# Optimization experiments

Hardware: AMD Instinct MI355X
Metric: run time of the kernel (lower is better)

Reference implementation:

```python
import jax, jax.numpy as jnp
import numpy as np
from jax import lax

L, B, T_IMG, T_TXT = 12, 2, 256, 64
E, H, G = 1024, 16, 2730
V = 16416  # image_vocab_count + 1
C = E // H
EPS = 1e-6  # flax LayerNorm default


def _ln(x, scale, bias):
    mu = jnp.mean(x, -1, keepdims=True)
    var = jnp.var(x, -1, keepdims=True)
    y = (x - mu) * lax.rsqrt(var + EPS)
    if scale is not None:
        y = y * scale
    if bias is not None:
        y = y + bias
    return y


def _attend(k, v, q, mask, o_w):
    # k,v: [B,K,H,C]  q: [B,Q,H,C]  mask: [B,K]
    bias = jnp.where(mask, 0.0, -jnp.inf)[:, None, None, :]
    w = jnp.einsum('bqhc,bkhc->bhqk', q, k) + bias
    w = jax.nn.softmax(w, axis=-1)
    out = jnp.einsum('bhqk,bkhc->bqhc', w, v)
    return out.reshape(out.shape[0], out.shape[1], E) @ o_w


def setup_inputs():
    key = jax.random.key(0)
    ks = jax.random.split(key, 16)
    s = 0.02
    n = lambda k, shape: jax.random.normal(k, shape, jnp.float32) * s
    return dict(
        encoder_state=n(ks[0], (B, T_TXT, E)),
        keys_state=jnp.zeros((L, B, T_IMG, H, C), jnp.float32),
        values_state=jnp.zeros((L, B, T_IMG, H, C), jnp.float32),
        attention_mask=jnp.ones((B, T_TXT), jnp.bool_),
        prev_token=5000,
        token_index=100,
        embed_tok=n(ks[1], (V, E)),
        embed_pos=n(ks[2], (T_IMG, E)),
        ln_emb_s=jnp.ones((E,), jnp.float32),
        ln_emb_b=jnp.zeros((E,), jnp.float32),
        final_ln_b=jnp.zeros((E,), jnp.float32),
        lm_head_w=n(ks[3], (E, V)),
        pre_sa_ln_b=jnp.zeros((L, E), jnp.float32),
        sa_q_w=n(ks[4], (L, E, E)), sa_k_w=n(ks[5], (L, E, E)),
        sa_v_w=n(ks[6], (L, E, E)), sa_o_w=n(ks[7], (L, E, E)),
        sa_ln_s=jnp.ones((L, E), jnp.float32), sa_ln_b=jnp.zeros((L, E), jnp.float32),
        pre_ca_ln_b=jnp.zeros((L, E), jnp.float32),
        ca_q_w=n(ks[8], (L, E, E)), ca_k_w=n(ks[9], (L, E, E)),
        ca_v_w=n(ks[10], (L, E, E)), ca_o_w=n(ks[11], (L, E, E)),
        ca_ln_s=jnp.ones((L, E), jnp.float32), ca_ln_b=jnp.zeros((L, E), jnp.float32),
        glu_ln0_b=jnp.zeros((L, E), jnp.float32),
        glu_fc0_w=n(ks[12], (L, E, G)), glu_fc1_w=n(ks[13], (L, E, G)),
        glu_ln1_b=jnp.zeros((L, G), jnp.float32),
        glu_fc2_w=n(ks[14], (L, G, E)),
    )


def _decode_step(encoder_state, keys_state, values_state, attention_mask,
                 prev_token, token_index, embed_tok, embed_pos,
                 ln_emb_s, ln_emb_b, final_ln_b, lm_head_w, layer_params):
    ones = jnp.ones((B, 1), jnp.int32)
    ds = embed_tok[prev_token * ones] + embed_pos[token_index * ones]  # [B,1,E]
    ds = _ln(ds, ln_emb_s, ln_emb_b)
    self_mask = jnp.broadcast_to(jnp.arange(T_IMG) < token_index + 1, (B, T_IMG))
    scale = C ** 0.5

    def step(ds, xs):
        ks_l, vs_l, p = xs  # per-layer KV cache [B,T_IMG,H,C] and params
        (pre_sa_b, qw, kw, vw, ow, sa_s, sa_b,
         pre_ca_b, cqw, ckw, cvw, cow, ca_s, ca_b,
         g0b, f0, f1, g1b, f2) = p
        # --- self attention with KV-cache append ---
        residual = ds
        x = _ln(ds, None, pre_sa_b)
        ks_l = lax.dynamic_update_slice(ks_l, (x @ kw).reshape(B, 1, H, C), (0, token_index, 0, 0))
        vs_l = lax.dynamic_update_slice(vs_l, (x @ vw).reshape(B, 1, H, C), (0, token_index, 0, 0))
        q = (x @ qw).reshape(B, 1, H, C) / scale
        x = _attend(ks_l, vs_l, q, self_mask, ow)
        ds = residual + _ln(x, sa_s, sa_b)
        # --- cross attention over encoder state ---
        residual = ds
        x = _ln(ds, None, pre_ca_b)
        ek = (encoder_state @ ckw).reshape(B, T_TXT, H, C)
        ev = (encoder_state @ cvw).reshape(B, T_TXT, H, C)
        q = (x @ cqw).reshape(B, 1, H, C) / scale
        x = _attend(ek, ev, q, attention_mask, cow)
        ds = residual + _ln(x, ca_s, ca_b)
        # --- GLU FFN ---
        residual = ds
        z = _ln(ds, None, g0b)
        w = jax.nn.gelu(z @ f0, approximate=False)
        z = _ln(w * (z @ f1), None, g1b)
        ds = residual + z @ f2
        return ds, (ks_l, vs_l)

    ds, (keys_state, values_state) = lax.scan(step, ds, (keys_state, values_state, layer_params))
    ds = _ln(ds, None, final_ln_b)
    logits = ds @ lm_head_w  # [B,1,V]
    return logits, keys_state, values_state


def reference(encoder_state, keys_state, values_state, attention_mask, prev_token,
              token_index, embed_tok, embed_pos, ln_emb_s, ln_emb_b, final_ln_b,
              lm_head_w, pre_sa_ln_b, sa_q_w, sa_k_w, sa_v_w, sa_o_w, sa_ln_s,
              sa_ln_b, pre_ca_ln_b, ca_q_w, ca_k_w, ca_v_w, ca_o_w, ca_ln_s,
              ca_ln_b, glu_ln0_b, glu_fc0_w, glu_fc1_w, glu_ln1_b, glu_fc2_w):
    layer_params = (pre_sa_ln_b, sa_q_w, sa_k_w, sa_v_w, sa_o_w, sa_ln_s, sa_ln_b,
                    pre_ca_ln_b, ca_q_w, ca_k_w, ca_v_w, ca_o_w, ca_ln_s, ca_ln_b,
                    glu_ln0_b, glu_fc0_w, glu_fc1_w, glu_ln1_b, glu_fc2_w)
    return _decode_step(encoder_state, keys_state, values_state, attention_mask,
                        prev_token, token_index, embed_tok, embed_pos,
                        ln_emb_s, ln_emb_b, final_ln_b, lm_head_w, layer_params)
```

## Files before the change

kernel.cpp:

```cpp
#include <hip/hip_runtime.h>
#include <math.h>

#define LAYERS 12
#define EE 1024
#define GG 2730
#define VV 16416
#define EPS 1e-6f

#define OFF_DS 0
#define NSLOT 37
#define OFF_ACC (OFF_DS + NSLOT*2048)
#define ACC_STRIDE 28672
#define AQ 0
#define AK 2048
#define AV 4096
#define AY 6144
#define ASC 10240
#define AOUT 12288
#define AY2 14336
#define AA 16384
#define AB2 21844
#define ACC_TOTAL (LAYERS*ACC_STRIDE)
#define ZERO_FLOATS (NSLOT*2048 + ACC_TOTAL)

#define KVL 524288
#define KVB 262144

struct MegaP {
  const float* enc; const float* keys_in; const float* values_in;
  const int* maski; const int* pt; const int* ti;
  const float* tok; const float* pos; const float* ln_s; const float* ln_b;
  const float* final_b; const float* lm_w;
  const float* pre_sa_b; const float* saq; const float* sak; const float* sav;
  const float* sao; const float* sas; const float* sab;
  const float* pre_ca_b; const float* caq; const float* ckw; const float* cvw;
  const float* cao; const float* cas; const float* cab;
  const float* g0b; const float* f0; const float* f1; const float* g1b; const float* f2;
  float* logits; float* keys_out; float* values_out; float* ws;
};

__device__ __forceinline__ void red4(float* sm, float& a, float& b, float& c, float& d){
  #pragma unroll
  for(int o=32;o;o>>=1){ a+=__shfl_down(a,o); b+=__shfl_down(b,o); c+=__shfl_down(c,o); d+=__shfl_down(d,o); }
  int w=threadIdx.x>>6, l=threadIdx.x&63;
  __syncthreads();
  if(l==0){ sm[w]=a; sm[4+w]=b; sm[8+w]=c; sm[12+w]=d; }
  __syncthreads();
  a=sm[0]+sm[1]+sm[2]+sm[3]; b=sm[4]+sm[5]+sm[6]+sm[7];
  c=sm[8]+sm[9]+sm[10]+sm[11]; d=sm[12]+sm[13]+sm[14]+sm[15];
}

__device__ __forceinline__ void ln_stats_g(const float* v, int K, float* sm,
    float& mu0, float& rs0, float& mu1, float& rs1){
  float s0=0,q0=0,s1=0,q1=0;
  for(int i=threadIdx.x;i<K;i+=256){ float a=v[i], b=v[K+i]; s0+=a;q0+=a*a;s1+=b;q1+=b*b; }
  red4(sm,s0,q0,s1,q1);
  mu0=s0/K; mu1=s1/K;
  rs0=rsqrtf(fmaxf(q0/K-mu0*mu0,0.f)+EPS);
  rs1=rsqrtf(fmaxf(q1/K-mu1*mu1,0.f)+EPS);
}

__device__ __forceinline__ void ln_stats_l(float (*Ds)[1024], float* sm,
    float& mu0, float& rs0, float& mu1, float& rs1){
  float s0=0,q0=0,s1=0,q1=0;
  for(int i=threadIdx.x;i<EE;i+=256){ float a=Ds[0][i], b=Ds[1][i]; s0+=a;q0+=a*a;s1+=b;q1+=b*b; }
  red4(sm,s0,q0,s1,q1);
  mu0=s0/EE; mu1=s1/EE;
  rs0=rsqrtf(fmaxf(q0/EE-mu0*mu0,0.f)+EPS);
  rs1=rsqrtf(fmaxf(q1/EE-mu1*mu1,0.f)+EPS);
}

__device__ __forceinline__ void build_ds3(const float* dsi, const float* accL,
    const float* sasl, const float* sabl, const float* casl, const float* cabl,
    float (*Ds)[1024], float* sm){
  float mu0,rs0,mu1,rs1;
  ln_stats_g(accL+AY, EE, sm, mu0,rs0,mu1,rs1);
  for(int i=threadIdx.x;i<EE;i+=256){ float sc=sasl[i], bi=sabl[i];
    Ds[0][i]=dsi[i]    + (accL[AY+i]-mu0)*rs0*sc + bi;
    Ds[1][i]=dsi[EE+i] + (accL[AY+EE+i]-mu1)*rs1*sc + bi; }
  ln_stats_g(accL+AY2, EE, sm, mu0,rs0,mu1,rs1);
  for(int i=threadIdx.x;i<EE;i+=256){ float sc=casl[i], bi=cabl[i];
    Ds[0][i] += (accL[AY2+i]-mu0)*rs0*sc + bi;
    Ds[1][i] += (accL[AY2+EE+i]-mu1)*rs1*sc + bi; }
}

__global__ __launch_bounds__(256)
void k_prelude(MegaP p){
  __shared__ float ev[EE];
  __shared__ float sm[16];
  const int t=threadIdx.x;
  int ptv = p.pt[0], tiv = p.ti[0];
  float s0=0,q0=0,d1=0,d2=0;
  for(int i=t;i<EE;i+=256){ float v=p.tok[(size_t)ptv*EE+i]+p.pos[(size_t)tiv*EE+i]; ev[i]=v; s0+=v; q0+=v*v; }
  red4(sm,s0,q0,d1,d2);
  float mu=s0/EE, rs=rsqrtf(fmaxf(q0/EE-mu*mu,0.f)+EPS);
  float* ds0 = p.ws + OFF_DS;
  __syncthreads();
  for(int i=t;i<EE;i+=256){ float y=(ev[i]-mu)*rs*p.ln_s[i]+p.ln_b[i]; ds0[i]=y; ds0[EE+i]=y; }
}

__global__ __launch_bounds__(256)
void k_qkv(MegaP p, int l){
  __shared__ float Xs[2][1024];
  __shared__ float sm[16];
  const int t=threadIdx.x, bx=blockIdx.x, by=blockIdx.y;
  if (bx >= 12){
    int cb = (bx-12)*64 + by;
    #pragma unroll
    for(int j=0;j<4;j++){
      int idx4 = cb*1024 + j*256 + t;
      int kv = idx4 >> 17;
      int r4 = idx4 & 131071;
      size_t off = (size_t)l*KVL + (size_t)r4*4;
      float4 v = *(const float4*)((kv? p.values_in : p.keys_in) + off);
      *(float4*)((kv? p.values_out : p.keys_out) + off) = v;
    }
    return;
  }
  const float* dsi = p.ws + OFF_DS + (size_t)(3*l)*2048;
  float* accL = p.ws + OFF_ACC + (size_t)l*ACC_STRIDE;
  const size_t lE2=(size_t)l*EE*EE, lE=(size_t)l*EE;
  int c = bx*256 + t;
  int sel = c>>10, cc = c&1023;
  const float* W = (sel==0? p.saq : sel==1? p.sak : p.sav) + lE2;
  float* O = accL + (sel==0? AQ : sel==1? AK : AV);
  int k0 = by*16;
  const float* wp = W + (size_t)k0*EE + cc;
  float wr[16];
  #pragma unroll
  for(int k=0;k<16;k++) wr[k] = wp[(size_t)k*EE];
  float mu0,rs0,mu1,rs1;
  ln_stats_g(dsi, EE, sm, mu0,rs0,mu1,rs1);
  for(int i=t;i<EE;i+=256){ float bi=p.pre_sa_b[lE+i];
    Xs[0][i]=(dsi[i]-mu0)*rs0+bi; Xs[1][i]=(dsi[EE+i]-mu1)*rs1+bi; }
  __syncthreads();
  float a0=0,a1=0;
  #pragma unroll
  for(int k=0;k<16;k++){ a0+=Xs[0][k0+k]*wr[k]; a1+=Xs[1][k0+k]*wr[k]; }
  atomicAdd(&O[cc],a0); atomicAdd(&O[EE+cc],a1);
}

__global__ __launch_bounds__(256)
void k_selfo(MegaP p, int l){
  __shared__ float Ds[2][1024];
  __shared__ float att[2][256];
  __shared__ float sm[16];
  const int t=threadIdx.x, bkid=blockIdx.x, tiv=p.ti[0];
  float* accL = p.ws + OFF_ACC + (size_t)l*ACC_STRIDE;
  const size_t lE2=(size_t)l*EE*EE;
  int cg=bkid&3, h=(bkid>>2)&15, sub=(bkid>>6)&3, hoff=h*64;
  if (t < 128){ int bb2=t>>6, c2=t&63; Ds[bb2][c2] = accL[AQ + bb2*EE + hoff + c2]*0.125f; }
  __syncthreads();
  for(int bb2=0;bb2<2;bb2++)
    for(int tt=t; tt<=tiv; tt+=256){
      const float* kr = (tt<tiv) ? (p.keys_in + (size_t)l*KVL + (size_t)bb2*KVB + (size_t)tt*EE + hoff)
                                 : (accL + AK + bb2*EE + hoff);
      float d=0;
      #pragma unroll
      for(int c2=0;c2<64;c2++) d += Ds[bb2][c2]*kr[c2];
      att[bb2][tt] = d;
    }
  __syncthreads();
  int wv=t>>6, l2=t&63;
  if (wv<2){
    float m=-3.4e38f;
    for(int tt=l2; tt<=tiv; tt+=64) m=fmaxf(m, att[wv][tt]);
    #pragma unroll
    for(int o=32;o;o>>=1) m=fmaxf(m,__shfl_xor(m,o));
    float s=0;
    for(int tt=l2; tt<=tiv; tt+=64){ float e=__expf(att[wv][tt]-m); att[wv][tt]=e; s+=e; }
    #pragma unroll
    for(int o=32;o;o>>=1) s+=__shfl_xor(s,o);
    if(l2==0) sm[8+wv]=1.f/s;
  }
  __syncthreads();
  {
    int bb2=t>>7, j=(t>>3)&15, part=t&7, colh=sub*16+j;
    float v=0;
    for(int tt=part; tt<=tiv; tt+=8){
      float vv = (tt<tiv)? p.values_in[(size_t)l*KVL + (size_t)bb2*KVB + (size_t)tt*EE + hoff + colh]
                         : accL[AV + bb2*EE + hoff + colh];
      v += att[bb2][tt]*vv;
    }
    v += __shfl_down(v,4,8); v += __shfl_down(v,2,8); v += __shfl_down(v,1,8);
    if(part==0) Ds[bb2][512+j] = v*sm[8+bb2];
  }
  __syncthreads();
  {
    int c = cg*256+t, kb = hoff + sub*16;
    const float* wp = p.sao + lE2 + (size_t)kb*EE + c;
    float a0=0,a1=0;
    #pragma unroll
    for(int j2=0;j2<16;j2++){ float w=wp[(size_t)j2*EE]; a0+=Ds[0][512+j2]*w; a1+=Ds[1][512+j2]*w; }
    atomicAdd(&accL[AY+c],a0); atomicAdd(&accL[AY+EE+c],a1);
  }
  if (cg==0 && sub==0){
    int bb2=t>>7, kv=(t>>6)&1, c2=t&63;
    float val = accL[(kv?AV:AK) + bb2*EE + hoff + c2];
    float* dst = (kv? p.values_out : p.keys_out)
               + (size_t)l*KVL + (size_t)bb2*KVB + (size_t)tiv*EE + hoff + c2;
    *dst = val;
  }
}

__global__ __launch_bounds__(256)
void k_qscore(MegaP p, int l){
  __shared__ float Xs[1024];
  __shared__ float P[16][64];
  __shared__ float qs[64];
  __shared__ float us[256];
  __shared__ float sm[16];
  const int t=threadIdx.x, bh=blockIdx.x, ec=blockIdx.y;
  const int b=bh>>4, h=bh&15, hoff=h*64;
  float* accL = p.ws + OFF_ACC + (size_t)l*ACC_STRIDE;
  const float* dsi = p.ws + OFF_DS + (size_t)(3*l)*2048;
  const size_t lE2=(size_t)l*EE*EE, lE=(size_t)l*EE;
  const int w=t>>6, ln=t&63;

  float s0=0,q0=0;
  for(int i=t;i<EE;i+=256){ float v=accL[AY+b*EE+i]; s0+=v; q0+=v*v; }
  #pragma unroll
  for(int o=32;o;o>>=1){ s0+=__shfl_down(s0,o); q0+=__shfl_down(q0,o); }
  if(ln==0){ sm[w]=s0; sm[4+w]=q0; }
  __syncthreads();
  float mu=(sm[0]+sm[1]+sm[2]+sm[3])/EE;
  float qq=(sm[4]+sm[5]+sm[6]+sm[7])/EE;
  float rs=rsqrtf(fmaxf(qq-mu*mu,0.f)+EPS);
  float s1=0,q1=0;
  for(int i=t;i<EE;i+=256){
    float d = dsi[b*EE+i] + (accL[AY+b*EE+i]-mu)*rs*p.sas[lE+i] + p.sab[lE+i];
    Xs[i]=d; s1+=d; q1+=d*d;
  }
  #pragma unroll
  for(int o=32;o;o>>=1){ s1+=__shfl_down(s1,o); q1+=__shfl_down(q1,o); }
  if(ln==0){ sm[8+w]=s1; sm[12+w]=q1; }
  __syncthreads();
  float mu2=(sm[8]+sm[9]+sm[10]+sm[11])/EE;
  float q2=(sm[12]+sm[13]+sm[14]+sm[15])/EE;
  float rs2=rsqrtf(fmaxf(q2-mu2*mu2,0.f)+EPS);
  for(int i=t;i<EE;i+=256) Xs[i] = (Xs[i]-mu2)*rs2 + p.pre_ca_b[lE+i];
  __syncthreads();

  {
    int c4=t&15, kr=t>>4;
    const float4* cq = (const float4*)(p.caq + lE2 + (size_t)kr*EE + hoff) + c4;
    float ax=0,ay=0,az=0,aw=0;
    #pragma unroll 8
    for(int i=0;i<64;i++){
      float4 wv = cq[(size_t)i*16*256];
      float x = Xs[kr+16*i];
      ax+=x*wv.x; ay+=x*wv.y; az+=x*wv.z; aw+=x*wv.w;
    }
    P[kr][c4*4+0]=ax; P[kr][c4*4+1]=ay; P[kr][c4*4+2]=az; P[kr][c4*4+3]=aw;
  }
  __syncthreads();
  if (t<64){
    float qv=0;
    #pragma unroll
    for(int kr=0;kr<16;kr++) qv += P[kr][t];
    qs[t] = qv*0.125f;
  }
  __syncthreads();

  {
    const float4* ckp = (const float4*)(p.ckw + lE2 + (size_t)(ec*256+t)*EE + hoff);
    float u=0;
    #pragma unroll
    for(int j=0;j<16;j++){
      float4 wv=ckp[j];
      u += wv.x*qs[4*j] + wv.y*qs[4*j+1] + wv.z*qs[4*j+2] + wv.w*qs[4*j+3];
    }
    us[t]=u;
  }
  __syncthreads();

  int t2=t&63, q4=t>>6;
  const float4* ep = (const float4*)(p.enc + (size_t)(b*64+t2)*EE + ec*256 + q4*64);
  float pa=0;
  #pragma unroll
  for(int j=0;j<16;j++){
    float4 e4=ep[j];
    pa += e4.x*us[q4*64+4*j] + e4.y*us[q4*64+4*j+1] + e4.z*us[q4*64+4*j+2] + e4.w*us[q4*64+4*j+3];
  }
  atomicAdd(&accL[ASC + (b*16+h)*64 + t2], pa);
}

__global__ __launch_bounds__(256)
void k_ov(MegaP p, int l){
  __shared__ float att[64];
  __shared__ float ctxp[2][128];
  __shared__ float ctxs[128];
  __shared__ float smr[2];
  const int t=threadIdx.x, bh=blockIdx.x, es=blockIdx.y;
  const int b=bh>>4, h=bh&15, hoff=h*64, e0=es*128;
  float* accL = p.ws + OFF_ACC + (size_t)l*ACC_STRIDE;
  const size_t lE2=(size_t)l*EE*EE;
  const int c=t&63, part=t>>6;
  const float* vp = p.cvw + lE2 + (size_t)(e0+part*32)*EE + hoff + c;
  float wr[32];
  #pragma unroll
  for(int j=0;j<32;j++) wr[j] = vp[(size_t)j*EE];
  if (t<64){
    float sc = accL[ASC + (b*16+h)*64 + t];
    int mi=b*64+t;
    bool valid = (p.maski[mi]!=0) || (((const unsigned char*)p.maski)[mi]!=0);
    sc = valid? sc : -3.4e38f;
    float m=sc;
    #pragma unroll
    for(int o=32;o;o>>=1) m=fmaxf(m,__shfl_xor(m,o));
    float e_ = valid? __expf(sc-m) : 0.f;
    float s=e_;
    #pragma unroll
    for(int o=32;o;o>>=1) s+=__shfl_xor(s,o);
    att[t]=e_;
    if(t==0) smr[0]=1.f/s;
  }
  __syncthreads();
  {
    int e2=t>>1, half=t&1;
    const float* ep = p.enc + (size_t)(b*64+half*32)*EE + e0+e2;
    float ca=0;
    #pragma unroll 8
    for(int tt=0;tt<32;tt++) ca += att[half*32+tt]*ep[(size_t)tt*EE];
    ctxp[half][e2]=ca;
  }
  __syncthreads();
  if (t<128) ctxs[t] = (ctxp[0][t]+ctxp[1][t])*smr[0];
  __syncthreads();
  float a=0;
  #pragma unroll
  for(int j=0;j<32;j++) a += ctxs[part*32+j]*wr[j];
  atomicAdd(&accL[AOUT + b*EE + hoff + c], a);
}

__global__ __launch_bounds__(256)
void k_y2(MegaP p, int l){
  __shared__ float Xs[2][1024];
  const int t=threadIdx.x;
  float* accL = p.ws + OFF_ACC + (size_t)l*ACC_STRIDE;
  const size_t lE2=(size_t)l*EE*EE;
  int c = blockIdx.x*256 + t;
  int k0 = blockIdx.y*16;
  const float* wp = p.cao + lE2 + (size_t)k0*EE + c;
  float wr[16];
  #pragma unroll
  for(int k=0;k<16;k++) wr[k] = wp[(size_t)k*EE];
  for(int i=t;i<EE;i+=256){ Xs[0][i]=accL[AOUT+i]; Xs[1][i]=accL[AOUT+EE+i]; }
  __syncthreads();
  float a0=0,a1=0;
  #pragma unroll
  for(int k=0;k<16;k++){ a0+=Xs[0][k0+k]*wr[k]; a1+=Xs[1][k0+k]*wr[k]; }
  atomicAdd(&accL[AY2+c],a0); atomicAdd(&accL[AY2+EE+c],a1);
}

__global__ __launch_bounds__(256)
void k_glu01(MegaP p, int l){
  __shared__ float Xs[2][1024];
  __shared__ float Ds[2][1024];
  __shared__ float sm[16];
  const int t=threadIdx.x;
  const float* dsi = p.ws + OFF_DS + (size_t)(3*l)*2048;
  float* accL = p.ws + OFF_ACC + (size_t)l*ACC_STRIDE;
  const size_t lEG=(size_t)l*EE*GG, lE=(size_t)l*EE;
  int c2 = blockIdx.x*256 + t;
  int k0 = blockIdx.y*16;
  int sel=0, col=0;
  const float* W = nullptr;
  float2 wr[16];
  if (c2 < 2730){
    sel = (c2>=1365); int cc2 = sel? c2-1365 : c2; col = cc2*2;
    W = (sel? p.f1 : p.f0) + lEG;
    const float2* wp = (const float2*)(W + (size_t)k0*GG + col);
    #pragma unroll
    for(int k=0;k<16;k++) wr[k] = wp[(size_t)k*1365];
  }
  build_ds3(dsi, accL, p.sas+lE, p.sab+lE, p.cas+lE, p.cab+lE, Ds, sm);
  float mu0,rs0,mu1,rs1;
  ln_stats_l(Ds, sm, mu0,rs0,mu1,rs1);
  for(int i=t;i<EE;i+=256){ float bi=p.g0b[lE+i];
    Xs[0][i]=(Ds[0][i]-mu0)*rs0+bi; Xs[1][i]=(Ds[1][i]-mu1)*rs1+bi; }
  __syncthreads();
  if (c2 < 2730){
    float* O = accL + (sel? AB2 : AA);
    float a0=0,a1=0,b0=0,b1=0;
    #pragma unroll
    for(int k=0;k<16;k++){
      float x0=Xs[0][k0+k], x1=Xs[1][k0+k];
      a0+=x0*wr[k].x; a1+=x0*wr[k].y; b0+=x1*wr[k].x; b1+=x1*wr[k].y;
    }
    atomicAdd(&O[col+0],a0); atomicAdd(&O[col+1],a1);
    atomicAdd(&O[GG+col+0],b0); atomicAdd(&O[GG+col+1],b1);
  }
}

__global__ __launch_bounds__(256)
void k_glu2(MegaP p, int l){
  __shared__ float Xs[2][2736];
  __shared__ float Ds[2][1024];
  __shared__ float sm[16];
  const int t=threadIdx.x;
  const float* dsi = p.ws + OFF_DS + (size_t)(3*l)*2048;
  float* ds4 = p.ws + OFF_DS + (size_t)(3*l+3)*2048;
  float* accL = p.ws + OFF_ACC + (size_t)l*ACC_STRIDE;
  const size_t lGE=(size_t)l*GG*EE, lE=(size_t)l*EE, lG=(size_t)l*GG;
  const int ks = blockIdx.y;
  int c = blockIdx.x*256 + t;
  int k0 = ks*32, k1 = k0+32; if (k1>GG) k1=GG;
  const float* wp = p.f2 + lGE + (size_t)k0*EE + c;
  float wr[32];
  #pragma unroll
  for(int k=0;k<32;k++) wr[k] = (k0+k<GG) ? wp[(size_t)k*EE] : 0.f;
  if (ks==0) build_ds3(dsi, accL, p.sas+lE, p.sab+lE, p.cas+lE, p.cab+lE, Ds, sm);
  float s0=0,q0=0,s1=0,q1=0;
  for(int i=t;i<GG;i+=256){
    float a0v=accL[AA+i], a1v=accL[AA+GG+i];
    float b0v=accL[AB2+i], b1v=accL[AB2+GG+i];
    float g0v=0.5f*a0v*(1.f+erff(a0v*0.70710678118654752f));
    float g1v=0.5f*a1v*(1.f+erff(a1v*0.70710678118654752f));
    float t0=g0v*b0v, t1=g1v*b1v;
    Xs[0][i]=t0; Xs[1][i]=t1;
    s0+=t0;q0+=t0*t0;s1+=t1;q1+=t1*t1;
  }
  red4(sm,s0,q0,s1,q1);
  float mu0=s0/GG, mu1=s1/GG;
  float rs0=rsqrtf(fmaxf(q0/GG-mu0*mu0,0.f)+EPS), rs1=rsqrtf(fmaxf(q1/GG-mu1*mu1,0.f)+EPS);
  for(int i=t;i<GG;i+=256){ float bi=p.g1b[lG+i];
    Xs[0][i]=(Xs[0][i]-mu0)*rs0+bi; Xs[1][i]=(Xs[1][i]-mu1)*rs1+bi; }
  __syncthreads();
  float a0=0,b0=0;
  if (ks==0){ a0=Ds[0][c]; b0=Ds[1][c]; }
  #pragma unroll
  for(int k=0;k<32;k++){
    if (k0+k<GG){ a0+=Xs[0][k0+k]*wr[k]; b0+=Xs[1][k0+k]*wr[k]; }
  }
  atomicAdd(&ds4[c],a0); atomicAdd(&ds4[EE+c],b0);
}

__global__ __launch_bounds__(256)
void k_lm(MegaP p){
  __shared__ float Xs[2][1024];
  __shared__ float sm[16];
  const int t=threadIdx.x;
  const float* dsf = p.ws + OFF_DS + (size_t)36*2048;
  float mu0,rs0,mu1,rs1;
  ln_stats_g(dsf, EE, sm, mu0,rs0,mu1,rs1);
  for(int i=t;i<EE;i+=256){ float bi=p.final_b[i];
    Xs[0][i]=(dsf[i]-mu0)*rs0+bi; Xs[1][i]=(dsf[EE+i]-mu1)*rs1+bi; }
  __syncthreads();
  int c4 = blockIdx.x*256 + t;
  if (c4 < 4104){
    int col = c4*4;
    int k0 = blockIdx.y*32;
    const float4* wp = (const float4*)(p.lm_w + (size_t)k0*VV + col);
    float a0=0,a1=0,a2=0,a3=0,b0=0,b1=0,b2=0,b3=0;
    #pragma unroll 8
    for(int k=0;k<32;k++){
      float4 w=*wp; wp+=4104;
      float x0=Xs[0][k0+k], x1=Xs[1][k0+k];
      a0+=x0*w.x; a1+=x0*w.y; a2+=x0*w.z; a3+=x0*w.w;
      b0+=x1*w.x; b1+=x1*w.y; b2+=x1*w.z; b3+=x1*w.w;
    }
    atomicAdd(&p.logits[col+0],a0); atomicAdd(&p.logits[col+1],a1);
    atomicAdd(&p.logits[col+2],a2); atomicAdd(&p.logits[col+3],a3);
    atomicAdd(&p.logits[VV+col+0],b0); atomicAdd(&p.logits[VV+col+1],b1);
    atomicAdd(&p.logits[VV+col+2],b2); atomicAdd(&p.logits[VV+col+3],b3);
  }
}

extern "C" void kernel_launch(void* const* d_in, const int* in_sizes, int n_in,
                              void* d_out, int out_size, void* d_ws, size_t ws_size,
                              hipStream_t stream){
  (void)in_sizes; (void)n_in; (void)out_size; (void)ws_size;
  float* out = (float*)d_out;
  float* ws = (float*)d_ws;

  MegaP P;
  P.enc        = (const float*)d_in[0];
  P.keys_in    = (const float*)d_in[1];
  P.values_in  = (const float*)d_in[2];
  P.maski      = (const int*)d_in[3];
  P.pt         = (const int*)d_in[4];
  P.ti         = (const int*)d_in[5];
  P.tok        = (const float*)d_in[6];
  P.pos        = (const float*)d_in[7];
  P.ln_s       = (const float*)d_in[8];
  P.ln_b       = (const float*)d_in[9];
  P.final_b    = (const float*)d_in[10];
  P.lm_w       = (const float*)d_in[11];
  P.pre_sa_b   = (const float*)d_in[12];
  P.saq        = (const float*)d_in[13];
  P.sak        = (const float*)d_in[14];
  P.sav        = (const float*)d_in[15];
  P.sao        = (const float*)d_in[16];
  P.sas        = (const float*)d_in[17];
  P.sab        = (const float*)d_in[18];
  P.pre_ca_b   = (const float*)d_in[19];
  P.caq        = (const float*)d_in[20];
  P.ckw        = (const float*)d_in[21];
  P.cvw        = (const float*)d_in[22];
  P.cao        = (const float*)d_in[23];
  P.cas        = (const float*)d_in[24];
  P.cab        = (const float*)d_in[25];
  P.g0b        = (const float*)d_in[26];
  P.f0         = (const float*)d_in[27];
  P.f1         = (const float*)d_in[28];
  P.g1b        = (const float*)d_in[29];
  P.f2         = (const float*)d_in[30];
  P.logits     = out;
  P.keys_out   = out + (size_t)2*VV;
  P.values_out = P.keys_out + (size_t)LAYERS*KVL;
  P.ws         = ws;

  hipMemsetAsync(ws + OFF_DS, 0, (size_t)ZERO_FLOATS*sizeof(float), stream);
  hipMemsetAsync(P.logits, 0, (size_t)2*VV*sizeof(float), stream);

  k_prelude<<<1,256,0,stream>>>(P);
  for (int l=0;l<LAYERS;l++){
    k_qkv   <<<dim3(16,64),256,0,stream>>>(P,l);
    k_selfo <<<256,        256,0,stream>>>(P,l);
    k_qscore<<<dim3(32,4), 256,0,stream>>>(P,l);
    k_ov    <<<dim3(32,8), 256,0,stream>>>(P,l);
    k_y2    <<<dim3(4,64), 256,0,stream>>>(P,l);
    k_glu01 <<<dim3(11,64),256,0,stream>>>(P,l);
    k_glu2  <<<dim3(4,86), 256,0,stream>>>(P,l);
  }
  k_lm<<<dim3(17,32),256,0,stream>>>(P);
}
```

Measured before the change: 1.075 ms.

## Fuse cross-attention output projection into ov kernel and replace memsets with in-kernel zeroing

Merges the k_ov and k_y2 kernels. Each (batch, head, E-slice) block now reduces its partial head context and multiplies it directly by that head's 64 rows of the cross-attention output weight, accumulating into AY2 with atomics. This drops the AOUT intermediate and one launch per layer. The two host memsets are also removed: the prelude kernel zeroes logits and the first layer's accumulators, and the qkv copy blocks zero the next layer's accumulator and ds slot. In exchange, each head's output-weight slice is re-read by 16 blocks, and each block issues 1024 atomic adds.

```diff
diff --git a/kernel.cpp b/kernel.cpp
--- a/kernel.cpp
+++ b/kernel.cpp
@@ -16,12 +16,10 @@
 #define AV 4096
 #define AY 6144
 #define ASC 10240
-#define AOUT 12288
 #define AY2 14336
 #define AA 16384
 #define AB2 21844
 #define ACC_TOTAL (LAYERS*ACC_STRIDE)
-#define ZERO_FLOATS (NSLOT*2048 + ACC_TOTAL)
 
 #define KVL 524288
 #define KVB 262144
@@ -88,15 +86,24 @@
 void k_prelude(MegaP p){
   __shared__ float ev[EE];
   __shared__ float sm[16];
-  const int t=threadIdx.x;
-  int ptv = p.pt[0], tiv = p.ti[0];
-  float s0=0,q0=0,d1=0,d2=0;
-  for(int i=t;i<EE;i+=256){ float v=p.tok[(size_t)ptv*EE+i]+p.pos[(size_t)tiv*EE+i]; ev[i]=v; s0+=v; q0+=v*v; }
-  red4(sm,s0,q0,d1,d2);
-  float mu=s0/EE, rs=rsqrtf(fmaxf(q0/EE-mu*mu,0.f)+EPS);
-  float* ds0 = p.ws + OFF_DS;
-  __syncthreads();
-  for(int i=t;i<EE;i+=256){ float y=(ev[i]-mu)*rs*p.ln_s[i]+p.ln_b[i]; ds0[i]=y; ds0[EE+i]=y; }
+  const int t=threadIdx.x, b=blockIdx.x;
+  if (b==0){
+    int ptv = p.pt[0], tiv = p.ti[0];
+    float s0=0,q0=0,d1=0,d2=0;
+    for(int i=t;i<EE;i+=256){ float v=p.tok[(size_t)ptv*EE+i]+p.pos[(size_t)tiv*EE+i]; ev[i]=v; s0+=v; q0+=v*v; }
+    red4(sm,s0,q0,d1,d2);
+    float mu=s0/EE, rs=rsqrtf(fmaxf(q0/EE-mu*mu,0.f)+EPS);
+    float* ds0 = p.ws + OFF_DS;
+    __syncthreads();
+    for(int i=t;i<EE;i+=256){ float y=(ev[i]-mu)*rs*p.ln_s[i]+p.ln_b[i]; ds0[i]=y; ds0[EE+i]=y; }
+  } else {
+    int idx = (b-1)*256 + t;
+    for (int i=idx; i<2*VV; i+=9984) p.logits[i]=0.f;
+    float* a0 = p.ws + OFF_ACC;
+    for (int i=idx; i<ACC_STRIDE; i+=9984) a0[i]=0.f;
+    float* d3 = p.ws + OFF_DS + 3*2048;
+    for (int i=idx; i<2048; i+=9984) d3[i]=0.f;
+  }
 }
 
 __global__ __launch_bounds__(256)
@@ -114,6 +121,13 @@
       size_t off = (size_t)l*KVL + (size_t)r4*4;
       float4 v = *(const float4*)((kv? p.values_in : p.keys_in) + off);
       *(float4*)((kv? p.values_out : p.keys_out) + off) = v;
+    }
+    if (l < 11){
+      int zi = cb*256 + t;
+      float* an = p.ws + OFF_ACC + (size_t)(l+1)*ACC_STRIDE;
+      if (zi < ACC_STRIDE) an[zi]=0.f;
+      float* dn = p.ws + OFF_DS + (size_t)(3*l+6)*2048;
+      if (zi < 2048) dn[zi]=0.f;
     }
     return;
   }
@@ -286,11 +300,12 @@
 }
 
 __global__ __launch_bounds__(256)
-void k_ov(MegaP p, int l){
+void k_ovy2(MegaP p, int l){
   __shared__ float att[64];
   __shared__ float ctxp[2][128];
   __shared__ float ctxs[128];
-  __shared__ float smr[2];
+  __shared__ float P[256];
+  __shared__ float outh[64];
   const int t=threadIdx.x, bh=blockIdx.x, es=blockIdx.y;
   const int b=bh>>4, h=bh&15, hoff=h*64, e0=es*128;
   float* accL = p.ws + OFF_ACC + (size_t)l*ACC_STRIDE;
@@ -312,8 +327,7 @@
     float s=e_;
     #pragma unroll
     for(int o=32;o;o>>=1) s+=__shfl_xor(s,o);
-    att[t]=e_;
-    if(t==0) smr[0]=1.f/s;
+    att[t]=e_/s;
   }
   __syncthreads();
   {
@@ -325,32 +339,26 @@
     ctxp[half][e2]=ca;
   }
   __syncthreads();
-  if (t<128) ctxs[t] = (ctxp[0][t]+ctxp[1][t])*smr[0];
-  __syncthreads();
-  float a=0;
-  #pragma unroll
-  for(int j=0;j<32;j++) a += ctxs[part*32+j]*wr[j];
-  atomicAdd(&accL[AOUT + b*EE + hoff + c], a);
-}
-
-__global__ __launch_bounds__(256)
-void k_y2(MegaP p, int l){
-  __shared__ float Xs[2][1024];
-  const int t=threadIdx.x;
-  float* accL = p.ws + OFF_ACC + (size_t)l*ACC_STRIDE;
-  const size_t lE2=(size_t)l*EE*EE;
-  int c = blockIdx.x*256 + t;
-  int k0 = blockIdx.y*16;
-  const float* wp = p.cao + lE2 + (size_t)k0*EE + c;
-  float wr[16];
-  #pragma unroll
-  for(int k=0;k<16;k++) wr[k] = wp[(size_t)k*EE];
-  for(int i=t;i<EE;i+=256){ Xs[0][i]=accL[AOUT+i]; Xs[1][i]=accL[AOUT+EE+i]; }
-  __syncthreads();
-  float a0=0,a1=0;
-  #pragma unroll
-  for(int k=0;k<16;k++){ a0+=Xs[0][k0+k]*wr[k]; a1+=Xs[1][k0+k]*wr[k]; }
-  atomicAdd(&accL[AY2+c],a0); atomicAdd(&accL[AY2+EE+c],a1);
+  if (t<128) ctxs[t] = ctxp[0][t]+ctxp[1][t];
+  __syncthreads();
+  {
+    float po=0;
+    #pragma unroll
+    for(int j=0;j<32;j++) po += ctxs[part*32+j]*wr[j];
+    P[t]=po;
+  }
+  __syncthreads();
+  if (t<64) outh[t] = P[t]+P[64+t]+P[128+t]+P[192+t];
+  __syncthreads();
+  {
+    const float* cop = p.cao + lE2 + (size_t)hoff*EE;
+    for(int n=t;n<EE;n+=256){
+      float y=0;
+      #pragma unroll 8
+      for(int c2=0;c2<64;c2++) y += outh[c2]*cop[(size_t)c2*EE + n];
+      atomicAdd(&accL[AY2 + b*EE + n], y);
+    }
+  }
 }
 
 __global__ __launch_bounds__(256)
@@ -511,16 +519,12 @@
   P.values_out = P.keys_out + (size_t)LAYERS*KVL;
   P.ws         = ws;
 
-  hipMemsetAsync(ws + OFF_DS, 0, (size_t)ZERO_FLOATS*sizeof(float), stream);
-  hipMemsetAsync(P.logits, 0, (size_t)2*VV*sizeof(float), stream);
-
-  k_prelude<<<1,256,0,stream>>>(P);
+  k_prelude<<<40,256,0,stream>>>(P);
   for (int l=0;l<LAYERS;l++){
     k_qkv   <<<dim3(16,64),256,0,stream>>>(P,l);
     k_selfo <<<256,        256,0,stream>>>(P,l);
     k_qscore<<<dim3(32,4), 256,0,stream>>>(P,l);
-    k_ov    <<<dim3(32,8), 256,0,stream>>>(P,l);
-    k_y2    <<<dim3(4,64), 256,0,stream>>>(P,l);
+    k_ovy2  <<<dim3(32,8), 256,0,stream>>>(P,l);
     k_glu01 <<<dim3(11,64),256,0,stream>>>(P,l);
     k_glu2  <<<dim3(4,86), 256,0,stream>>>(P,l);
   }
```

Measured after the change: 1.237 ms. +15.1%, slower.
